# Performance work log

Hardware: AMD Instinct MI355X
Metric: run time of the kernel (lower is better)

The kernel has to match this reference:

```python
import jax, jax.numpy as jnp
import numpy as np

B, S, D, E, K = 4, 4096, 4096, 64, 8


def setup_inputs() -> dict:
    key = jax.random.key(0)
    k1, k2, k3, k4, k5, k6 = jax.random.split(key, 6)
    lim = 1.0 / np.sqrt(D)
    return {
        "x": jax.random.normal(k1, (B, S, D), dtype=jnp.float32),
        "noise": jax.random.normal(k2, (B, S, E), dtype=jnp.float32),
        "W_route": jax.random.uniform(k3, (D, E), jnp.float32, -lim, lim),
        "b_route": jax.random.uniform(k4, (E,), jnp.float32, -lim, lim),
        "W_noise": jax.random.uniform(k5, (D, E), jnp.float32, -lim, lim),
        "b_noise": jax.random.uniform(k6, (E,), jnp.float32, -lim, lim),
    }


def reference(x, noise, W_route, b_route, W_noise, b_noise):
    # routing logits: [B,S,E]
    logits = jnp.einsum("bsd,de->bse", x, W_route) + b_route
    noise_logits = jnp.einsum("bsd,de->bse", x, W_noise) + b_noise
    logits = logits + noise * jax.nn.softplus(noise_logits)
    probs = jax.nn.softmax(logits, axis=-1)
    top_k_probs, selected_experts = jax.lax.top_k(probs, K)  # [B,S,K]
    weighted = top_k_probs / jnp.sum(top_k_probs, axis=-1, keepdims=True)
    return weighted, selected_experts, probs
```

## Files before the change

### kernel.cpp

```cpp
#include <hip/hip_runtime.h>
#include <math.h>
#include <stdint.h>

#define NTOK 16384
#define KD   4096
#define EDIM 64
#define MT   64
#define KC   64
#define NC   (KD / KC)
#define WSTR 132
#define XSTR 68
#define WOFF 0
#define XOFF (KC * WSTR)
#define SMEMF (XOFF + MT * XSTR)

__global__ __launch_bounds__(512, 2)
void router_fused(const float* __restrict__ x,
                  const float* __restrict__ noise,
                  const float* __restrict__ Wr,
                  const float* __restrict__ br,
                  const float* __restrict__ Wn,
                  const float* __restrict__ bn,
                  float* __restrict__ out) {
    __shared__ float smem[SMEMF];
    const int tid = threadIdx.x;
    const int t0 = blockIdx.x * MT;

    const int eb = (tid & 31) * 4;
    const int tb = (tid >> 5) * 4;

    const int xr = tid >> 3;
    const int xq = (tid & 7) * 8;
    const int wk = tid >> 3;
    const int wc = (tid & 7) * 16;
    const float* xsrc = x + (size_t)(t0 + xr) * KD + xq;
    const float* wsrc = (wc < 64) ? (Wr + (size_t)wk * EDIM + wc)
                                  : (Wn + (size_t)wk * EDIM + (wc - 64));

    float acc[4][4];
#pragma unroll
    for (int i = 0; i < 4; ++i)
#pragma unroll
        for (int j = 0; j < 4; ++j) acc[i][j] = 0.f;

    float4 px0 = *(const float4*)(xsrc);
    float4 px1 = *(const float4*)(xsrc + 4);
    float4 pw0 = *(const float4*)(wsrc);
    float4 pw1 = *(const float4*)(wsrc + 4);
    float4 pw2 = *(const float4*)(wsrc + 8);
    float4 pw3 = *(const float4*)(wsrc + 12);
    {
        float* xd = &smem[XOFF + xr * XSTR + xq];
        *(float4*)xd = px0; *(float4*)(xd + 4) = px1;
        float* wd = &smem[WOFF + wk * WSTR + wc];
        *(float4*)wd = pw0; *(float4*)(wd + 4) = pw1;
        *(float4*)(wd + 8) = pw2; *(float4*)(wd + 12) = pw3;
    }

    for (int c = 0; c < NC; ++c) {
        __syncthreads();
        const bool pre = (c + 1) < NC;
        if (pre) {
            const size_t ko = (size_t)(c + 1) * KC;
            px0 = *(const float4*)(xsrc + ko);
            px1 = *(const float4*)(xsrc + ko + 4);
            const float* wp = wsrc + ko * EDIM;
            pw0 = *(const float4*)(wp);
            pw1 = *(const float4*)(wp + 4);
            pw2 = *(const float4*)(wp + 8);
            pw3 = *(const float4*)(wp + 12);
        }

#pragma unroll 4
        for (int kk = 0; kk < KC; kk += 4) {
            float xv[4][4];
#pragma unroll
            for (int i = 0; i < 4; ++i)
                *(float4*)xv[i] = *(const float4*)&smem[XOFF + (tb + i) * XSTR + kk];
            float wv[4][4];
#pragma unroll
            for (int kp = 0; kp < 4; ++kp)
                *(float4*)wv[kp] = *(const float4*)&smem[WOFF + (kk + kp) * WSTR + eb];
#pragma unroll
            for (int i = 0; i < 4; ++i)
#pragma unroll
                for (int j = 0; j < 4; ++j) {
                    acc[i][j] = fmaf(xv[i][0], wv[0][j], acc[i][j]);
                    acc[i][j] = fmaf(xv[i][1], wv[1][j], acc[i][j]);
                    acc[i][j] = fmaf(xv[i][2], wv[2][j], acc[i][j]);
                    acc[i][j] = fmaf(xv[i][3], wv[3][j], acc[i][j]);
                }
        }

        __syncthreads();
        if (pre) {
            float* xd = &smem[XOFF + xr * XSTR + xq];
            *(float4*)xd = px0; *(float4*)(xd + 4) = px1;
            float* wd = &smem[WOFF + wk * WSTR + wc];
            *(float4*)wd = pw0; *(float4*)(wd + 4) = pw1;
            *(float4*)(wd + 8) = pw2; *(float4*)(wd + 12) = pw3;
        }
    }

#pragma unroll
    for (int i = 0; i < 4; ++i)
        *(float4*)&smem[(tb + i) * WSTR + eb] = *(float4*)acc[i];
    __syncthreads();

    const int wvid = tid >> 6;
    const int lane = tid & 63;
    const float brl = br[lane], bnl = bn[lane];
    for (int it = 0; it < 8; ++it) {
        const int tl = wvid * 8 + it;
        const int tg = t0 + tl;
        float v  = smem[tl * WSTR + lane] + brl;
        float nz = smem[tl * WSTR + 64 + lane] + bnl;
        float sp = log1pf(expf(-fabsf(nz))) + fmaxf(nz, 0.f);
        v += noise[(size_t)tg * EDIM + lane] * sp;

        float mx = v;
#pragma unroll
        for (int o = 32; o >= 1; o >>= 1) mx = fmaxf(mx, __shfl_xor(mx, o, 64));
        float p = expf(v - mx);
        float sm = p;
#pragma unroll
        for (int o = 32; o >= 1; o >>= 1) sm += __shfl_xor(sm, o, 64);
        float prob = p / sm;
        out[(size_t)NTOK * 16 + (size_t)tg * EDIM + lane] = prob;

        float pv = prob;
        float wvals[8]; int widx[8]; float tsum = 0.f;
#pragma unroll
        for (int j = 0; j < 8; ++j) {
            float bv = pv; int bi = lane;
#pragma unroll
            for (int o = 32; o >= 1; o >>= 1) {
                float ov = __shfl_xor(bv, o, 64);
                int   oi = __shfl_xor(bi, o, 64);
                if (ov > bv || (ov == bv && oi < bi)) { bv = ov; bi = oi; }
            }
            wvals[j] = bv; widx[j] = bi; tsum += bv;
            if (lane == bi) pv = -1.0f;
        }
        if (lane < 8) {
            float myw = wvals[0]; int myi = widx[0];
#pragma unroll
            for (int j = 1; j < 8; ++j) if (lane == j) { myw = wvals[j]; myi = widx[j]; }
            out[(size_t)tg * 8 + lane] = myw / tsum;
            out[(size_t)NTOK * 8 + (size_t)tg * 8 + lane] = (float)myi;
        }
    }
}

extern "C" void kernel_launch(void* const* d_in, const int* in_sizes, int n_in,
                              void* d_out, int out_size, void* d_ws, size_t ws_size,
                              hipStream_t stream) {
    const float* x     = (const float*)d_in[0];
    const float* noise = (const float*)d_in[1];
    const float* Wr    = (const float*)d_in[2];
    const float* br    = (const float*)d_in[3];
    const float* Wn    = (const float*)d_in[4];
    const float* bn    = (const float*)d_in[5];
    float* out = (float*)d_out;
    hipLaunchKernelGGL(router_fused, dim3(NTOK / MT), dim3(512), 0, stream,
                       x, noise, Wr, br, Wn, bn, out);
}
```

Baseline: 576.6 us.

## Restructure router GEMM: lane-per-token with wave-uniform weight loads from global

The GEMM mapping changes so each lane owns one token and each wave owns 16 expert columns. The weights are read straight from global memory with wave-uniform addresses (scalar or broadcast loads) instead of being staged in LDS. Only x is staged, transposed into a double-buffered padded LDS tile with a larger K chunk, which drops one barrier per chunk. The intent is to cut LDS traffic and synchronization per FMA. The risks are bank-conflicted scalar transpose stores and a weight-load latency that sits on the critical path.

```diff
diff --git a/kernel.cpp b/kernel.cpp
--- a/kernel.cpp
+++ b/kernel.cpp
@@ -6,13 +6,12 @@
 #define KD   4096
 #define EDIM 64
 #define MT   64
-#define KC   64
+#define KC   128
 #define NC   (KD / KC)
-#define WSTR 132
-#define XSTR 68
-#define WOFF 0
-#define XOFF (KC * WSTR)
-#define SMEMF (XOFF + MT * XSTR)
+#define XTS  65
+#define BUFF (KC * XTS)
+#define LSTR 132
+#define SMEMF (2 * BUFF + 4 * XTS)
 
 __global__ __launch_bounds__(512, 2)
 void router_fused(const float* __restrict__ x,
@@ -23,98 +22,136 @@
                   const float* __restrict__ bn,
                   float* __restrict__ out) {
     __shared__ float smem[SMEMF];
-    const int tid = threadIdx.x;
-    const int t0 = blockIdx.x * MT;
-
-    const int eb = (tid & 31) * 4;
-    const int tb = (tid >> 5) * 4;
-
-    const int xr = tid >> 3;
-    const int xq = (tid & 7) * 8;
-    const int wk = tid >> 3;
-    const int wc = (tid & 7) * 16;
-    const float* xsrc = x + (size_t)(t0 + xr) * KD + xq;
-    const float* wsrc = (wc < 64) ? (Wr + (size_t)wk * EDIM + wc)
-                                  : (Wn + (size_t)wk * EDIM + (wc - 64));
-
-    float acc[4][4];
-#pragma unroll
-    for (int i = 0; i < 4; ++i)
-#pragma unroll
-        for (int j = 0; j < 4; ++j) acc[i][j] = 0.f;
-
-    float4 px0 = *(const float4*)(xsrc);
-    float4 px1 = *(const float4*)(xsrc + 4);
-    float4 pw0 = *(const float4*)(wsrc);
-    float4 pw1 = *(const float4*)(wsrc + 4);
-    float4 pw2 = *(const float4*)(wsrc + 8);
-    float4 pw3 = *(const float4*)(wsrc + 12);
+    const int tid  = threadIdx.x;
+    const int t0   = blockIdx.x * MT;
+    const int lane = tid & 63;
+
+    const int wv = __builtin_amdgcn_readfirstlane(tid >> 6);
+    const float* __restrict__ Wsel = (wv < 4) ? Wr : Wn;
+    const int c0 = (wv & 3) * 16;
+
+    const int sc = (tid & 31) * 4;
+    const int sr = tid >> 5;
+    const float* xsrc = x + (size_t)(t0 + sr) * KD + sc;
+
+    float acc[16];
+#pragma unroll
+    for (int j = 0; j < 16; ++j) acc[j] = 0.f;
+
+    float4 pf0 = *(const float4*)(xsrc);
+    float4 pf1 = *(const float4*)(xsrc + (size_t)16 * KD);
+    float4 pf2 = *(const float4*)(xsrc + (size_t)32 * KD);
+    float4 pf3 = *(const float4*)(xsrc + (size_t)48 * KD);
     {
-        float* xd = &smem[XOFF + xr * XSTR + xq];
-        *(float4*)xd = px0; *(float4*)(xd + 4) = px1;
-        float* wd = &smem[WOFF + wk * WSTR + wc];
-        *(float4*)wd = pw0; *(float4*)(wd + 4) = pw1;
-        *(float4*)(wd + 8) = pw2; *(float4*)(wd + 12) = pw3;
-    }
+        float* d = smem;
+#pragma unroll
+        for (int i = 0; i < 4; ++i) {
+            d[(sc + i) * XTS + sr     ] = (&pf0.x)[i];
+            d[(sc + i) * XTS + sr + 16] = (&pf1.x)[i];
+            d[(sc + i) * XTS + sr + 32] = (&pf2.x)[i];
+            d[(sc + i) * XTS + sr + 48] = (&pf3.x)[i];
+        }
+    }
+
+#define FMA16(xc, u0, u1, u2, u3) do { \
+        acc[ 0] = fmaf(xc, u0.x, acc[ 0]); \
+        acc[ 1] = fmaf(xc, u0.y, acc[ 1]); \
+        acc[ 2] = fmaf(xc, u0.z, acc[ 2]); \
+        acc[ 3] = fmaf(xc, u0.w, acc[ 3]); \
+        acc[ 4] = fmaf(xc, u1.x, acc[ 4]); \
+        acc[ 5] = fmaf(xc, u1.y, acc[ 5]); \
+        acc[ 6] = fmaf(xc, u1.z, acc[ 6]); \
+        acc[ 7] = fmaf(xc, u1.w, acc[ 7]); \
+        acc[ 8] = fmaf(xc, u2.x, acc[ 8]); \
+        acc[ 9] = fmaf(xc, u2.y, acc[ 9]); \
+        acc[10] = fmaf(xc, u2.z, acc[10]); \
+        acc[11] = fmaf(xc, u2.w, acc[11]); \
+        acc[12] = fmaf(xc, u3.x, acc[12]); \
+        acc[13] = fmaf(xc, u3.y, acc[13]); \
+        acc[14] = fmaf(xc, u3.z, acc[14]); \
+        acc[15] = fmaf(xc, u3.w, acc[15]); \
+    } while (0)
 
     for (int c = 0; c < NC; ++c) {
         __syncthreads();
         const bool pre = (c + 1) < NC;
         if (pre) {
-            const size_t ko = (size_t)(c + 1) * KC;
-            px0 = *(const float4*)(xsrc + ko);
-            px1 = *(const float4*)(xsrc + ko + 4);
-            const float* wp = wsrc + ko * EDIM;
-            pw0 = *(const float4*)(wp);
-            pw1 = *(const float4*)(wp + 4);
-            pw2 = *(const float4*)(wp + 8);
-            pw3 = *(const float4*)(wp + 12);
-        }
-
-#pragma unroll 4
-        for (int kk = 0; kk < KC; kk += 4) {
-            float xv[4][4];
-#pragma unroll
-            for (int i = 0; i < 4; ++i)
-                *(float4*)xv[i] = *(const float4*)&smem[XOFF + (tb + i) * XSTR + kk];
-            float wv[4][4];
-#pragma unroll
-            for (int kp = 0; kp < 4; ++kp)
-                *(float4*)wv[kp] = *(const float4*)&smem[WOFF + (kk + kp) * WSTR + eb];
-#pragma unroll
-            for (int i = 0; i < 4; ++i)
-#pragma unroll
-                for (int j = 0; j < 4; ++j) {
-                    acc[i][j] = fmaf(xv[i][0], wv[0][j], acc[i][j]);
-                    acc[i][j] = fmaf(xv[i][1], wv[1][j], acc[i][j]);
-                    acc[i][j] = fmaf(xv[i][2], wv[2][j], acc[i][j]);
-                    acc[i][j] = fmaf(xv[i][3], wv[3][j], acc[i][j]);
-                }
-        }
-
-        __syncthreads();
+            const float* xs = xsrc + (size_t)(c + 1) * KC;
+            pf0 = *(const float4*)(xs);
+            pf1 = *(const float4*)(xs + (size_t)16 * KD);
+            pf2 = *(const float4*)(xs + (size_t)32 * KD);
+            pf3 = *(const float4*)(xs + (size_t)48 * KD);
+        }
+
+        const float* xt  = smem + (c & 1) * BUFF + lane;
+        const float* wr_ = Wsel + c0 + (size_t)c * KC * EDIM;
+
+        float4 wa0 = *(const float4*)(wr_ + 0);
+        float4 wa1 = *(const float4*)(wr_ + 4);
+        float4 wa2 = *(const float4*)(wr_ + 8);
+        float4 wa3 = *(const float4*)(wr_ + 12);
+        float4 wb0 = *(const float4*)(wr_ + EDIM + 0);
+        float4 wb1 = *(const float4*)(wr_ + EDIM + 4);
+        float4 wb2 = *(const float4*)(wr_ + EDIM + 8);
+        float4 wb3 = *(const float4*)(wr_ + EDIM + 12);
+        float xa = xt[0];
+        float xb = xt[XTS];
+
+#pragma unroll 2
+        for (int kk = 0; kk < KC; kk += 2) {
+            const float  xca = xa;
+            const float4 ua0 = wa0, ua1 = wa1, ua2 = wa2, ua3 = wa3;
+            if (kk + 2 < KC) {
+                const float* nw = wr_ + (size_t)(kk + 2) * EDIM;
+                wa0 = *(const float4*)(nw + 0);
+                wa1 = *(const float4*)(nw + 4);
+                wa2 = *(const float4*)(nw + 8);
+                wa3 = *(const float4*)(nw + 12);
+                xa  = xt[(kk + 2) * XTS];
+            }
+            FMA16(xca, ua0, ua1, ua2, ua3);
+
+            const float  xcb = xb;
+            const float4 ub0 = wb0, ub1 = wb1, ub2 = wb2, ub3 = wb3;
+            if (kk + 3 < KC) {
+                const float* nw = wr_ + (size_t)(kk + 3) * EDIM;
+                wb0 = *(const float4*)(nw + 0);
+                wb1 = *(const float4*)(nw + 4);
+                wb2 = *(const float4*)(nw + 8);
+                wb3 = *(const float4*)(nw + 12);
+                xb  = xt[(kk + 3) * XTS];
+            }
+            FMA16(xcb, ub0, ub1, ub2, ub3);
+        }
+
         if (pre) {
-            float* xd = &smem[XOFF + xr * XSTR + xq];
-            *(float4*)xd = px0; *(float4*)(xd + 4) = px1;
-            float* wd = &smem[WOFF + wk * WSTR + wc];
-            *(float4*)wd = pw0; *(float4*)(wd + 4) = pw1;
-            *(float4*)(wd + 8) = pw2; *(float4*)(wd + 12) = pw3;
-        }
-    }
-
-#pragma unroll
-    for (int i = 0; i < 4; ++i)
-        *(float4*)&smem[(tb + i) * WSTR + eb] = *(float4*)acc[i];
+            float* d = smem + ((c + 1) & 1) * BUFF;
+#pragma unroll
+            for (int i = 0; i < 4; ++i) {
+                d[(sc + i) * XTS + sr     ] = (&pf0.x)[i];
+                d[(sc + i) * XTS + sr + 16] = (&pf1.x)[i];
+                d[(sc + i) * XTS + sr + 32] = (&pf2.x)[i];
+                d[(sc + i) * XTS + sr + 48] = (&pf3.x)[i];
+            }
+        }
+    }
+
     __syncthreads();
+#pragma unroll
+    for (int q = 0; q < 4; ++q) {
+        float4 v = make_float4(acc[q * 4 + 0], acc[q * 4 + 1],
+                               acc[q * 4 + 2], acc[q * 4 + 3]);
+        *(float4*)&smem[lane * LSTR + wv * 16 + q * 4] = v;
+    }
+    __syncthreads();
 
     const int wvid = tid >> 6;
-    const int lane = tid & 63;
     const float brl = br[lane], bnl = bn[lane];
     for (int it = 0; it < 8; ++it) {
         const int tl = wvid * 8 + it;
         const int tg = t0 + tl;
-        float v  = smem[tl * WSTR + lane] + brl;
-        float nz = smem[tl * WSTR + 64 + lane] + bnl;
+        float v  = smem[tl * LSTR + lane] + brl;
+        float nz = smem[tl * LSTR + 64 + lane] + bnl;
         float sp = log1pf(expf(-fabsf(nz))) + fmaxf(nz, 0.f);
         v += noise[(size_t)tg * EDIM + lane] * sp;
 
```

After: 921.9 us. 1.6x slower.

## Stream weights from global into registers and double-buffer swizzled x tiles

Applied to the files above, without the earlier changes.

Rewrites the GEMM main loop so W_route/W_noise columns are loaded straight from global (L2-resident) into registers with software prefetch, instead of being staged through shared memory. Shared memory now holds only x tiles, double-buffered with an XOR swizzle to avoid bank conflicts, with a larger K chunk that halves the number of barriers. This is meant to cut LDS traffic and synchronisation. In exchange, each wave now re-reads the weights from cache every K step, and the prefetch pointer clamping adds some complexity.

```diff
diff --git a/kernel.cpp b/kernel.cpp
--- a/kernel.cpp
+++ b/kernel.cpp
@@ -6,13 +6,29 @@
 #define KD   4096
 #define EDIM 64
 #define MT   64
-#define KC   64
+#define KC   128
 #define NC   (KD / KC)
-#define WSTR 132
-#define XSTR 68
-#define WOFF 0
-#define XOFF (KC * WSTR)
-#define SMEMF (XOFF + MT * XSTR)
+#define BUFF (MT * KC)
+#define LSTR 132
+
+#define FMAG(xv, w0, w1, w2, w3, a) do {                          \
+        a[0] = fmaf(xv.x, w0.x, a[0]);                            \
+        a[0] = fmaf(xv.y, w1.x, a[0]);                            \
+        a[0] = fmaf(xv.z, w2.x, a[0]);                            \
+        a[0] = fmaf(xv.w, w3.x, a[0]);                            \
+        a[1] = fmaf(xv.x, w0.y, a[1]);                            \
+        a[1] = fmaf(xv.y, w1.y, a[1]);                            \
+        a[1] = fmaf(xv.z, w2.y, a[1]);                            \
+        a[1] = fmaf(xv.w, w3.y, a[1]);                            \
+        a[2] = fmaf(xv.x, w0.z, a[2]);                            \
+        a[2] = fmaf(xv.y, w1.z, a[2]);                            \
+        a[2] = fmaf(xv.z, w2.z, a[2]);                            \
+        a[2] = fmaf(xv.w, w3.z, a[2]);                            \
+        a[3] = fmaf(xv.x, w0.w, a[3]);                            \
+        a[3] = fmaf(xv.y, w1.w, a[3]);                            \
+        a[3] = fmaf(xv.z, w2.w, a[3]);                            \
+        a[3] = fmaf(xv.w, w3.w, a[3]);                            \
+    } while (0)
 
 __global__ __launch_bounds__(512, 2)
 void router_fused(const float* __restrict__ x,
@@ -22,20 +38,23 @@
                   const float* __restrict__ Wn,
                   const float* __restrict__ bn,
                   float* __restrict__ out) {
-    __shared__ float smem[SMEMF];
-    const int tid = threadIdx.x;
-    const int t0 = blockIdx.x * MT;
-
-    const int eb = (tid & 31) * 4;
-    const int tb = (tid >> 5) * 4;
-
-    const int xr = tid >> 3;
-    const int xq = (tid & 7) * 8;
-    const int wk = tid >> 3;
-    const int wc = (tid & 7) * 16;
-    const float* xsrc = x + (size_t)(t0 + xr) * KD + xq;
-    const float* wsrc = (wc < 64) ? (Wr + (size_t)wk * EDIM + wc)
-                                  : (Wn + (size_t)wk * EDIM + (wc - 64));
+    __shared__ float smem[2 * BUFF];
+    const int tid  = threadIdx.x;
+    const int t0   = blockIdx.x * MT;
+    const int lane = tid & 63;
+    const int wv   = tid >> 6;
+    const int tg   = (tid >> 2) & 15;
+    const int cg   = tid & 3;
+    const int sw   = tg & 7;
+
+    const float* __restrict__ Wsel = (wv < 4) ? Wr : Wn;
+    const float* wbase = Wsel + ((wv & 3) * 16 + cg * 4);
+
+    const int srow = tid >> 3;
+    const int skq  = (tid & 7) * 16;
+    const int sc0  = skq >> 2;
+    const int ssw  = (srow >> 2) & 7;
+    const float* xsrc = x + (size_t)(t0 + srow) * KD + skq;
 
     float acc[4][4];
 #pragma unroll
@@ -43,80 +62,109 @@
 #pragma unroll
         for (int j = 0; j < 4; ++j) acc[i][j] = 0.f;
 
-    float4 px0 = *(const float4*)(xsrc);
-    float4 px1 = *(const float4*)(xsrc + 4);
-    float4 pw0 = *(const float4*)(wsrc);
-    float4 pw1 = *(const float4*)(wsrc + 4);
-    float4 pw2 = *(const float4*)(wsrc + 8);
-    float4 pw3 = *(const float4*)(wsrc + 12);
     {
-        float* xd = &smem[XOFF + xr * XSTR + xq];
-        *(float4*)xd = px0; *(float4*)(xd + 4) = px1;
-        float* wd = &smem[WOFF + wk * WSTR + wc];
-        *(float4*)wd = pw0; *(float4*)(wd + 4) = pw1;
-        *(float4*)(wd + 8) = pw2; *(float4*)(wd + 12) = pw3;
-    }
-
+        float4 s0 = *(const float4*)(xsrc);
+        float4 s1 = *(const float4*)(xsrc + 4);
+        float4 s2 = *(const float4*)(xsrc + 8);
+        float4 s3 = *(const float4*)(xsrc + 12);
+        float* d = &smem[srow * KC];
+        *(float4*)&d[((sc0 + 0) ^ ssw) << 2] = s0;
+        *(float4*)&d[((sc0 + 1) ^ ssw) << 2] = s1;
+        *(float4*)&d[((sc0 + 2) ^ ssw) << 2] = s2;
+        *(float4*)&d[((sc0 + 3) ^ ssw) << 2] = s3;
+    }
+
+    const float* wlim = wbase + (size_t)1022 * 256;
+    const float* wpre = wbase + 512;
+    float4 wA0 = *(const float4*)(wbase +   0);
+    float4 wA1 = *(const float4*)(wbase +  64);
+    float4 wA2 = *(const float4*)(wbase + 128);
+    float4 wA3 = *(const float4*)(wbase + 192);
+    float4 wB0 = *(const float4*)(wbase + 256);
+    float4 wB1 = *(const float4*)(wbase + 320);
+    float4 wB2 = *(const float4*)(wbase + 384);
+    float4 wB3 = *(const float4*)(wbase + 448);
+
+    float4 s0, s1, s2, s3;
     for (int c = 0; c < NC; ++c) {
         __syncthreads();
         const bool pre = (c + 1) < NC;
         if (pre) {
-            const size_t ko = (size_t)(c + 1) * KC;
-            px0 = *(const float4*)(xsrc + ko);
-            px1 = *(const float4*)(xsrc + ko + 4);
-            const float* wp = wsrc + ko * EDIM;
-            pw0 = *(const float4*)(wp);
-            pw1 = *(const float4*)(wp + 4);
-            pw2 = *(const float4*)(wp + 8);
-            pw3 = *(const float4*)(wp + 12);
-        }
-
-#pragma unroll 4
-        for (int kk = 0; kk < KC; kk += 4) {
-            float xv[4][4];
-#pragma unroll
-            for (int i = 0; i < 4; ++i)
-                *(float4*)xv[i] = *(const float4*)&smem[XOFF + (tb + i) * XSTR + kk];
-            float wv[4][4];
-#pragma unroll
-            for (int kp = 0; kp < 4; ++kp)
-                *(float4*)wv[kp] = *(const float4*)&smem[WOFF + (kk + kp) * WSTR + eb];
-#pragma unroll
-            for (int i = 0; i < 4; ++i)
-#pragma unroll
-                for (int j = 0; j < 4; ++j) {
-                    acc[i][j] = fmaf(xv[i][0], wv[0][j], acc[i][j]);
-                    acc[i][j] = fmaf(xv[i][1], wv[1][j], acc[i][j]);
-                    acc[i][j] = fmaf(xv[i][2], wv[2][j], acc[i][j]);
-                    acc[i][j] = fmaf(xv[i][3], wv[3][j], acc[i][j]);
-                }
-        }
-
-        __syncthreads();
+            const float* xs = xsrc + (size_t)(c + 1) * KC;
+            s0 = *(const float4*)(xs);
+            s1 = *(const float4*)(xs + 4);
+            s2 = *(const float4*)(xs + 8);
+            s3 = *(const float4*)(xs + 12);
+        }
+
+        const char* xrb = (const char*)&smem[(c & 1) * BUFF + (tg << 2) * KC];
+
+        for (int gp = 0; gp < 16; ++gp) {
+            const int g = gp << 1;
+            const float* pA = wpre;
+            const float* pB = wpre + 256;
+            wpre += 512;
+            if (wpre > wlim) wpre = wlim;
+
+            const int offA = ((g ^ sw) << 4);
+            const int offB = (((g + 1) ^ sw) << 4);
+            float4 xa0 = *(const float4*)(xrb + offA);
+            float4 xa1 = *(const float4*)(xrb + offA + 512);
+            float4 xa2 = *(const float4*)(xrb + offA + 1024);
+            float4 xa3 = *(const float4*)(xrb + offA + 1536);
+            float4 xb0 = *(const float4*)(xrb + offB);
+            float4 xb1 = *(const float4*)(xrb + offB + 512);
+            float4 xb2 = *(const float4*)(xrb + offB + 1024);
+            float4 xb3 = *(const float4*)(xrb + offB + 1536);
+
+            FMAG(xa0, wA0, wA1, wA2, wA3, acc[0]);
+            FMAG(xa1, wA0, wA1, wA2, wA3, acc[1]);
+            FMAG(xa2, wA0, wA1, wA2, wA3, acc[2]);
+            FMAG(xa3, wA0, wA1, wA2, wA3, acc[3]);
+            wA0 = *(const float4*)(pA);
+            wA1 = *(const float4*)(pA + 64);
+            wA2 = *(const float4*)(pA + 128);
+            wA3 = *(const float4*)(pA + 192);
+
+            FMAG(xb0, wB0, wB1, wB2, wB3, acc[0]);
+            FMAG(xb1, wB0, wB1, wB2, wB3, acc[1]);
+            FMAG(xb2, wB0, wB1, wB2, wB3, acc[2]);
+            FMAG(xb3, wB0, wB1, wB2, wB3, acc[3]);
+            wB0 = *(const float4*)(pB);
+            wB1 = *(const float4*)(pB + 64);
+            wB2 = *(const float4*)(pB + 128);
+            wB3 = *(const float4*)(pB + 192);
+        }
+
         if (pre) {
-            float* xd = &smem[XOFF + xr * XSTR + xq];
-            *(float4*)xd = px0; *(float4*)(xd + 4) = px1;
-            float* wd = &smem[WOFF + wk * WSTR + wc];
-            *(float4*)wd = pw0; *(float4*)(wd + 4) = pw1;
-            *(float4*)(wd + 8) = pw2; *(float4*)(wd + 12) = pw3;
-        }
-    }
-
-#pragma unroll
-    for (int i = 0; i < 4; ++i)
-        *(float4*)&smem[(tb + i) * WSTR + eb] = *(float4*)acc[i];
+            float* d = &smem[((c + 1) & 1) * BUFF + srow * KC];
+            *(float4*)&d[((sc0 + 0) ^ ssw) << 2] = s0;
+            *(float4*)&d[((sc0 + 1) ^ ssw) << 2] = s1;
+            *(float4*)&d[((sc0 + 2) ^ ssw) << 2] = s2;
+            *(float4*)&d[((sc0 + 3) ^ ssw) << 2] = s3;
+        }
+    }
+
     __syncthreads();
+    {
+        const int colbase = ((wv & 4) << 4) + ((wv & 3) << 4) + (cg << 2);
+#pragma unroll
+        for (int i = 0; i < 4; ++i) {
+            float4 v = make_float4(acc[i][0], acc[i][1], acc[i][2], acc[i][3]);
+            *(float4*)&smem[((tg << 2) + i) * LSTR + colbase] = v;
+        }
+    }
+    __syncthreads();
 
     const int wvid = tid >> 6;
-    const int lane = tid & 63;
     const float brl = br[lane], bnl = bn[lane];
     for (int it = 0; it < 8; ++it) {
         const int tl = wvid * 8 + it;
-        const int tg = t0 + tl;
-        float v  = smem[tl * WSTR + lane] + brl;
-        float nz = smem[tl * WSTR + 64 + lane] + bnl;
+        const int tg_ = t0 + tl;
+        float v  = smem[tl * LSTR + lane] + brl;
+        float nz = smem[tl * LSTR + 64 + lane] + bnl;
         float sp = log1pf(expf(-fabsf(nz))) + fmaxf(nz, 0.f);
-        v += noise[(size_t)tg * EDIM + lane] * sp;
+        v += noise[(size_t)tg_ * EDIM + lane] * sp;
 
         float mx = v;
 #pragma unroll
@@ -126,7 +174,7 @@
 #pragma unroll
         for (int o = 32; o >= 1; o >>= 1) sm += __shfl_xor(sm, o, 64);
         float prob = p / sm;
-        out[(size_t)NTOK * 16 + (size_t)tg * EDIM + lane] = prob;
+        out[(size_t)NTOK * 16 + (size_t)tg_ * EDIM + lane] = prob;
 
         float pv = prob;
         float wvals[8]; int widx[8]; float tsum = 0.f;
@@ -146,8 +194,8 @@
             float myw = wvals[0]; int myi = widx[0];
 #pragma unroll
             for (int j = 1; j < 8; ++j) if (lane == j) { myw = wvals[j]; myi = widx[j]; }
-            out[(size_t)tg * 8 + lane] = myw / tsum;
-            out[(size_t)NTOK * 8 + (size_t)tg * 8 + lane] = (float)myi;
+            out[(size_t)tg_ * 8 + lane] = myw / tsum;
+            out[(size_t)NTOK * 8 + (size_t)tg_ * 8 + lane] = (float)myi;
         }
     }
 }
```

Result: slower. 736.5 us (+27.7%).

## Split K across wave groups with 8x8 register tiles and swizzled double-buffered LDS

Applied to the files above, without the earlier changes.

Splits the K dimension into four quarters, each handled by a pair of waves, and gives each thread an 8x8 accumulator tile instead of 4x4, which raises FMAs per LDS load. X is stored transposed and W with an XOR swizzle in double-buffered shared memory, so only one barrier pair is needed per stage. The four partial sums are reduced through LDS before the unchanged softmax/top-k epilogue. The larger accumulator tile raises register pressure under launch_bounds(512,2), and the transposed scalar X stores may cause LDS bank conflicts.

```diff
diff --git a/kernel.cpp b/kernel.cpp
--- a/kernel.cpp
+++ b/kernel.cpp
@@ -6,13 +6,27 @@
 #define KD   4096
 #define EDIM 64
 #define MT   64
-#define KC   64
-#define NC   (KD / KC)
-#define WSTR 132
-#define XSTR 68
-#define WOFF 0
-#define XOFF (KC * WSTR)
-#define SMEMF (XOFF + MT * XSTR)
+#define KQ   1024
+#define KC   16
+#define NS   (KQ / KC)
+#define QSTR 3072
+#define BSTR (4 * QSTR)
+#define PSTR 132
+#define PQ   (MT * PSTR)
+#define SMEMF (4 * PQ)
+
+#define LD4(p) (*(const float4*)(p))
+
+#define FMAK(xs, i) do { \
+    acc[i][0] = fmaf(xs, wa.x, acc[i][0]); \
+    acc[i][1] = fmaf(xs, wa.y, acc[i][1]); \
+    acc[i][2] = fmaf(xs, wa.z, acc[i][2]); \
+    acc[i][3] = fmaf(xs, wa.w, acc[i][3]); \
+    acc[i][4] = fmaf(xs, wb.x, acc[i][4]); \
+    acc[i][5] = fmaf(xs, wb.y, acc[i][5]); \
+    acc[i][6] = fmaf(xs, wb.z, acc[i][6]); \
+    acc[i][7] = fmaf(xs, wb.w, acc[i][7]); \
+  } while (0)
 
 __global__ __launch_bounds__(512, 2)
 void router_fused(const float* __restrict__ x,
@@ -23,100 +37,115 @@
                   const float* __restrict__ bn,
                   float* __restrict__ out) {
     __shared__ float smem[SMEMF];
-    const int tid = threadIdx.x;
-    const int t0 = blockIdx.x * MT;
+    const int tid  = threadIdx.x;
+    const int t0   = blockIdx.x * MT;
+    const int lane = tid & 63;
+    const int wv   = tid >> 6;
+    const int q    = wv >> 1;
+    const int m    = wv & 1;
+    const int tg   = lane >> 3;
+    const int cg   = lane & 7;
+    const int colb = m * 64 + cg * 8;
 
-    const int eb = (tid & 31) * 4;
-    const int tb = (tid >> 5) * 4;
+    const int sq    = tid >> 7;
+    const int st    = tid & 127;
+    const int stok  = st >> 1;
+    const int skc   = (st & 1) * 8;
+    const int skrow = st >> 3;
+    const int sseg  = st & 7;
+    const float* xsrc = x + (size_t)(t0 + stok) * KD + sq * KQ + skc;
+    const float* wsrc = (sseg < 4) ? (Wr + sseg * 16) : (Wn + (sseg - 4) * 16);
+    wsrc += (size_t)(sq * KQ + skrow) * EDIM;
+    const int wkey = (skrow & 7) << 2;
 
-    const int xr = tid >> 3;
-    const int xq = (tid & 7) * 8;
-    const int wk = tid >> 3;
-    const int wc = (tid & 7) * 16;
-    const float* xsrc = x + (size_t)(t0 + xr) * KD + xq;
-    const float* wsrc = (wc < 64) ? (Wr + (size_t)wk * EDIM + wc)
-                                  : (Wn + (size_t)wk * EDIM + (wc - 64));
+    float acc[8][8];
+#pragma unroll
+    for (int i = 0; i < 8; ++i)
+#pragma unroll
+        for (int j = 0; j < 8; ++j) acc[i][j] = 0.f;
 
-    float acc[4][4];
-#pragma unroll
-    for (int i = 0; i < 4; ++i)
-#pragma unroll
-        for (int j = 0; j < 4; ++j) acc[i][j] = 0.f;
+    float4 gx0, gx1, gw0, gw1, gw2, gw3;
 
-    float4 px0 = *(const float4*)(xsrc);
-    float4 px1 = *(const float4*)(xsrc + 4);
-    float4 pw0 = *(const float4*)(wsrc);
-    float4 pw1 = *(const float4*)(wsrc + 4);
-    float4 pw2 = *(const float4*)(wsrc + 8);
-    float4 pw3 = *(const float4*)(wsrc + 12);
-    {
-        float* xd = &smem[XOFF + xr * XSTR + xq];
-        *(float4*)xd = px0; *(float4*)(xd + 4) = px1;
-        float* wd = &smem[WOFF + wk * WSTR + wc];
-        *(float4*)wd = pw0; *(float4*)(wd + 4) = pw1;
-        *(float4*)(wd + 8) = pw2; *(float4*)(wd + 12) = pw3;
-    }
+#define GLOAD(s) do { \
+        const float* xp = xsrc + (s) * KC; \
+        gx0 = LD4(xp); gx1 = LD4(xp + 4); \
+        const float* wp = wsrc + (size_t)(s) * KC * EDIM; \
+        gw0 = LD4(wp); gw1 = LD4(wp + 4); gw2 = LD4(wp + 8); gw3 = LD4(wp + 12); \
+    } while (0)
 
-    for (int c = 0; c < NC; ++c) {
+#define XWRITE(b) do { \
+        float* xb_ = smem + (b) * BSTR + sq * QSTR; \
+        xb_[(skc + 0) * 64 + stok] = gx0.x; \
+        xb_[(skc + 1) * 64 + stok] = gx0.y; \
+        xb_[(skc + 2) * 64 + stok] = gx0.z; \
+        xb_[(skc + 3) * 64 + stok] = gx0.w; \
+        xb_[(skc + 4) * 64 + stok] = gx1.x; \
+        xb_[(skc + 5) * 64 + stok] = gx1.y; \
+        xb_[(skc + 6) * 64 + stok] = gx1.z; \
+        xb_[(skc + 7) * 64 + stok] = gx1.w; \
+        float* wb_ = xb_ + 1024; \
+        const int c0_ = sseg * 16; \
+        *(float4*)&wb_[skrow * 128 + ((c0_ +  0) ^ wkey)] = gw0; \
+        *(float4*)&wb_[skrow * 128 + ((c0_ +  4) ^ wkey)] = gw1; \
+        *(float4*)&wb_[skrow * 128 + ((c0_ +  8) ^ wkey)] = gw2; \
+        *(float4*)&wb_[skrow * 128 + ((c0_ + 12) ^ wkey)] = gw3; \
+    } while (0)
+
+    GLOAD(0);
+    XWRITE(0);
+
+    for (int s = 0; s < NS; ++s) {
         __syncthreads();
-        const bool pre = (c + 1) < NC;
-        if (pre) {
-            const size_t ko = (size_t)(c + 1) * KC;
-            px0 = *(const float4*)(xsrc + ko);
-            px1 = *(const float4*)(xsrc + ko + 4);
-            const float* wp = wsrc + ko * EDIM;
-            pw0 = *(const float4*)(wp);
-            pw1 = *(const float4*)(wp + 4);
-            pw2 = *(const float4*)(wp + 8);
-            pw3 = *(const float4*)(wp + 12);
-        }
+        if (s + 1 < NS) GLOAD(s + 1);
+
+        const float* xq = smem + (s & 1) * BSTR + q * QSTR;
+        const float* wq = xq + 1024;
 
 #pragma unroll 4
-        for (int kk = 0; kk < KC; kk += 4) {
-            float xv[4][4];
-#pragma unroll
-            for (int i = 0; i < 4; ++i)
-                *(float4*)xv[i] = *(const float4*)&smem[XOFF + (tb + i) * XSTR + kk];
-            float wv[4][4];
-#pragma unroll
-            for (int kp = 0; kp < 4; ++kp)
-                *(float4*)wv[kp] = *(const float4*)&smem[WOFF + (kk + kp) * WSTR + eb];
-#pragma unroll
-            for (int i = 0; i < 4; ++i)
-#pragma unroll
-                for (int j = 0; j < 4; ++j) {
-                    acc[i][j] = fmaf(xv[i][0], wv[0][j], acc[i][j]);
-                    acc[i][j] = fmaf(xv[i][1], wv[1][j], acc[i][j]);
-                    acc[i][j] = fmaf(xv[i][2], wv[2][j], acc[i][j]);
-                    acc[i][j] = fmaf(xv[i][3], wv[3][j], acc[i][j]);
-                }
+        for (int kk = 0; kk < KC; ++kk) {
+            float4 xa = LD4(&xq[kk * 64 + tg * 8]);
+            float4 xc = LD4(&xq[kk * 64 + tg * 8 + 4]);
+            const int key = (kk & 7) << 2;
+            float4 wa = LD4(&wq[kk * 128 + ((colb)     ^ key)]);
+            float4 wb = LD4(&wq[kk * 128 + ((colb + 4) ^ key)]);
+            FMAK(xa.x, 0); FMAK(xa.y, 1); FMAK(xa.z, 2); FMAK(xa.w, 3);
+            FMAK(xc.x, 4); FMAK(xc.y, 5); FMAK(xc.z, 6); FMAK(xc.w, 7);
         }
 
         __syncthreads();
-        if (pre) {
-            float* xd = &smem[XOFF + xr * XSTR + xq];
-            *(float4*)xd = px0; *(float4*)(xd + 4) = px1;
-            float* wd = &smem[WOFF + wk * WSTR + wc];
-            *(float4*)wd = pw0; *(float4*)(wd + 4) = pw1;
-            *(float4*)(wd + 8) = pw2; *(float4*)(wd + 12) = pw3;
+        if (s + 1 < NS) XWRITE((s + 1) & 1);
+    }
+
+    __syncthreads();
+    {
+        float* pq_ = smem + q * PQ;
+#pragma unroll
+        for (int i = 0; i < 8; ++i) {
+            *(float4*)&pq_[(tg * 8 + i) * PSTR + colb] =
+                make_float4(acc[i][0], acc[i][1], acc[i][2], acc[i][3]);
+            *(float4*)&pq_[(tg * 8 + i) * PSTR + colb + 4] =
+                make_float4(acc[i][4], acc[i][5], acc[i][6], acc[i][7]);
         }
     }
+    __syncthreads();
 
 #pragma unroll
-    for (int i = 0; i < 4; ++i)
-        *(float4*)&smem[(tb + i) * WSTR + eb] = *(float4*)acc[i];
+    for (int j = 0; j < 16; ++j) {
+        const int idx = tid + 512 * j;
+        const int tok = idx >> 7, col = idx & 127;
+        const int li  = tok * PSTR + col;
+        smem[li] = (smem[li] + smem[PQ + li]) + (smem[2 * PQ + li] + smem[3 * PQ + li]);
+    }
     __syncthreads();
 
-    const int wvid = tid >> 6;
-    const int lane = tid & 63;
     const float brl = br[lane], bnl = bn[lane];
     for (int it = 0; it < 8; ++it) {
-        const int tl = wvid * 8 + it;
-        const int tg = t0 + tl;
-        float v  = smem[tl * WSTR + lane] + brl;
-        float nz = smem[tl * WSTR + 64 + lane] + bnl;
+        const int tl  = wv * 8 + it;
+        const int tg_ = t0 + tl;
+        float v  = smem[tl * PSTR + lane] + brl;
+        float nz = smem[tl * PSTR + 64 + lane] + bnl;
         float sp = log1pf(expf(-fabsf(nz))) + fmaxf(nz, 0.f);
-        v += noise[(size_t)tg * EDIM + lane] * sp;
+        v += noise[(size_t)tg_ * EDIM + lane] * sp;
 
         float mx = v;
 #pragma unroll
@@ -126,7 +155,7 @@
 #pragma unroll
         for (int o = 32; o >= 1; o >>= 1) sm += __shfl_xor(sm, o, 64);
         float prob = p / sm;
-        out[(size_t)NTOK * 16 + (size_t)tg * EDIM + lane] = prob;
+        out[(size_t)NTOK * 16 + (size_t)tg_ * EDIM + lane] = prob;
 
         float pv = prob;
         float wvals[8]; int widx[8]; float tsum = 0.f;
@@ -146,8 +175,8 @@
             float myw = wvals[0]; int myi = widx[0];
 #pragma unroll
             for (int j = 1; j < 8; ++j) if (lane == j) { myw = wvals[j]; myi = widx[j]; }
-            out[(size_t)tg * 8 + lane] = myw / tsum;
-            out[(size_t)NTOK * 8 + (size_t)tg * 8 + lane] = (float)myi;
+            out[(size_t)tg_ * 8 + lane] = myw / tsum;
+            out[(size_t)NTOK * 8 + (size_t)tg_ * 8 + lane] = (float)myi;
         }
     }
 }
```

Result: faster. 557.4 us (-3.3%).
